# Performance work log

Measured on AMD Instinct MI355X. Metric: run time of the kernel, lower is better.

Reference implementation:

```python
import jax, jax.numpy as jnp
import numpy as np

B, C, H, W = 8, 128, 128, 128
PLANES, K, STRIDE, PAD = 128, 3, 1, 1
BN_EPS = 1e-5


def setup_inputs() -> dict:
    key = jax.random.key(0)
    k1, k2, k3, k4 = jax.random.split(key, 4)
    x = jax.random.normal(k1, (B, C, H, W), jnp.float32)
    # ConvOffset2D: Conv2d(C, 2C, 3, pad=1, bias=False), weights ~ N(0, 0.01)
    w_off = jax.random.normal(k2, (2 * C, C, 3, 3), jnp.float32) * 0.01
    w_conv = jax.random.normal(k3, (PLANES, C, K, K), jnp.float32) * 0.05
    b_conv = jax.random.normal(k4, (PLANES,), jnp.float32) * 0.01
    gamma = jnp.ones((PLANES,), jnp.float32)
    beta = jnp.zeros((PLANES,), jnp.float32)
    return {"x": x, "w_off": w_off, "w_conv": w_conv, "b_conv": b_conv,
            "gamma": gamma, "beta": beta}


def _conv2d(x, w, stride, pad):
    return jax.lax.conv_general_dilated(
        x, w, window_strides=(stride, stride),
        padding=[(pad, pad), (pad, pad)],
        dimension_numbers=("NCHW", "OIHW", "NCHW"))


def _deform_sample(x, offsets):
    """x: (B,C,H,W); offsets: (B,2C,H,W) -> bilinear offset-sampled (B,C,H,W).
    Faithful to ConvOffset2D: raw reshape (b,2c,h,w) -> (b*c, h*w, 2),
    coords = offsets + meshgrid(i,j), clamp, bilinear interp."""
    b, c, h, w = x.shape
    off = offsets.reshape(b * c, h * w, 2)              # quirky but faithful reshape
    grid = jnp.stack(jnp.meshgrid(jnp.arange(h, dtype=x.dtype),
                                  jnp.arange(w, dtype=x.dtype),
                                  indexing="ij"), axis=-1).reshape(1, h * w, 2)
    coords = off + grid                                  # (b*c, h*w, 2)
    yc = jnp.clip(coords[..., 0], 0.0, h - 1.0)
    xc = jnp.clip(coords[..., 1], 0.0, w - 1.0)
    y0, y1 = jnp.floor(yc), jnp.ceil(yc)
    x0, x1 = jnp.floor(xc), jnp.ceil(xc)
    img = x.reshape(b * c, h * w)

    def gather(yy, xx):
        idx = (yy * w + xx).astype(jnp.int32)
        return jnp.take_along_axis(img, idx, axis=1)

    v_lt = gather(y0, x0)
    v_rb = gather(y1, x1)
    v_lb = gather(y0, x1)
    v_rt = gather(y1, x0)
    dy = yc - y0
    dx = xc - x0
    v_t = v_lt + (v_rt - v_lt) * dy   # interp along height
    v_b = v_lb + (v_rb - v_lb) * dy
    out = v_t + (v_b - v_t) * dx      # interp along width
    return out.reshape(b, c, h, w)


def reference(x, w_off, w_conv, b_conv, gamma, beta):
    offsets = _conv2d(x, w_off, 1, 1)                    # (B, 2C, H, W)
    x_off = _deform_sample(x, offsets)                   # (B, C, H, W)
    y = _conv2d(x_off, w_conv, STRIDE, PAD) + b_conv[None, :, None, None]
    y = jax.nn.relu(y)
    # BatchNorm2d in training mode: batch statistics, biased variance
    mean = y.mean(axis=(0, 2, 3), keepdims=True)
    var = jnp.square(y - mean).mean(axis=(0, 2, 3), keepdims=True)
    y = (y - mean) * jax.lax.rsqrt(var + BN_EPS)
    return y * gamma[None, :, None, None] + beta[None, :, None, None]
```

## Files before the change

kernel.cpp:

```cpp
#include <hip/hip_runtime.h>

#define B_   8
#define C_   128
#define H_   128
#define W_   128
#define HW_  16384

typedef short v8s __attribute__((ext_vector_type(8)));
typedef float v4f __attribute__((ext_vector_type(4)));

#define ROWB 4160

__device__ __forceinline__ float bf2f(unsigned short u) {
  unsigned int v = ((unsigned int)u) << 16;
  float f; __builtin_memcpy(&f, &v, 4); return f;
}
__device__ __forceinline__ unsigned short f2us(float f) {
  unsigned int u; __builtin_memcpy(&u, &f, 4);
  u += 0x7fffu + ((u >> 16) & 1u);
  return (unsigned short)(u >> 16);
}

__global__ __launch_bounds__(256) void pack_w(const float* __restrict__ w,
                                              unsigned short* __restrict__ pack,
                                              uint4* __restrict__ zb, int G) {
  if (blockIdx.x == 0) zb[threadIdx.x] = (uint4){0u, 0u, 0u, 0u};
  int idx = blockIdx.x * 256 + threadIdx.x;
  if (idx >= 20480 * G) return;
  int j  = idx & 7;
  int l  = (idx >> 3) & 63;
  int g  = (idx >> 9) % G;
  int t2 = idx / (512 * G);
  int pp = t2 % 5;
  int cc = t2 / 5;
  int oc = g * 16 + (l & 15);
  int kk = ((l >> 4) << 3) + j;
  int ic = (cc << 4) + (kk & 15);
  int rs = pp * 2 + (kk >> 4);
  float v = (rs < 9) ? w[(oc * C_ + ic) * 9 + rs] : 0.f;
  pack[idx] = f2us(v);
}

__global__ __launch_bounds__(256) void transpose_x(const float* __restrict__ x,
                                                   unsigned short* __restrict__ xt) {
  __shared__ alignas(16) unsigned short t[32 * 132];
  const int j0 = blockIdx.x * 32, i = blockIdx.y, b = blockIdx.z;
  const int tid = threadIdx.x;
  for (int e = tid; e < 128 * 32; e += 256) {
    int c = e >> 5, jj = e & 31;
    float v = x[((b * C_ + c) * H_ + i) * W_ + j0 + jj];
    t[jj * 132 + c] = f2us(v);
  }
  __syncthreads();
  for (int f = tid; f < 1024; f += 256) {
    int cg = f >> 7, g = f & 127;
    int j = g >> 2, c4 = (g & 3) << 2;
    uint2 v = *(const uint2*)&t[j * 132 + cg * 16 + c4];
    *(uint2*)(xt + ((size_t)(b * 8 + cg) * HW_ + i * W_ + j0 + j) * 16 + c4) = v;
  }
}

template <int MODE, int G>
__global__ __launch_bounds__(256) void conv_gemm(const unsigned short* __restrict__ xt,
                                                 const unsigned short* __restrict__ pack,
                                                 const float* __restrict__ bias,
                                                 const char* __restrict__ zb,
                                                 unsigned short* __restrict__ outp,
                                                 float* __restrict__ ps) {
  __shared__ alignas(16) char rawb[3 * ROWB];
  __shared__ float bs1[128], bs2[128];

  const int nb = blockIdx.x;
  int b, i, mt;
  {
    int xcd = nb & 7, r = nb >> 3;
    if (MODE == 0) { b = r >> 5; mt = (r >> 4) & 1; i = xcd * 16 + (r & 15); }
    else           { b = r >> 4; mt = 0;            i = xcd * 16 + (r & 15); }
  }
  const int tid  = threadIdx.x;
  const int lane = tid & 63, wid = tid >> 6;
  const int q = lane >> 4, n = lane & 15;
  const int wm = wid & 1, wn = wid >> 1;

  if (MODE == 1 && tid < 128) { bs1[tid] = 0.f; bs2[tid] = 0.f; }
  if (tid < 12) {
    int r = tid >> 2, rem = tid & 3, side = rem >> 1, h = rem & 1;
    *(uint4*)(rawb + r * ROWB + (side ? 129 * 32 : 0) + h * 16) = (uint4){0u,0u,0u,0u};
  }

  int boff[5];
#pragma unroll
  for (int pp = 0; pp < 5; ++pp) {
    int rs = pp * 2 + (q >> 1);
    if (rs > 8) rs = 8;
    int r = (rs >= 6) ? 2 : ((rs >= 3) ? 1 : 0);
    int s = rs - r * 3;
    boff[pp] = r * ROWB + s * 32 + (q & 1) * 16;
  }
  const int pcol = (wn * 64 + n) * 32;

  v4f acc[4][4];
#pragma unroll
  for (int a = 0; a < 4; ++a)
#pragma unroll
    for (int c = 0; c < 4; ++c) acc[a][c] = (v4f){0.f, 0.f, 0.f, 0.f};

  const v8s* packv = (const v8s*)pack;
  const int gbase = mt * 8 + wm * 4;

  v8s Acur[4];
  {
    const v8s* ap = packv + (0 * G + gbase) * 64 + lane;
#pragma unroll
    for (int fm = 0; fm < 4; ++fm) Acur[fm] = ap[fm * 64];
  }

  for (int cc = 0; cc < 8; ++cc) {
    __syncthreads();
    const char* ccbase = (const char*)xt + (size_t)(b * 8 + cc) * (HW_ * 32);
#pragma unroll
    for (int t = 0; t < 3; ++t) {
      int c = wid * 3 + t, r = c >> 2, k = c & 3;
      int ii = i + r - 1;
      const char* src = ((unsigned)ii < 128u)
                          ? ccbase + ii * 4096 + k * 1024 + lane * 16
                          : zb + lane * 16;
      __builtin_amdgcn_global_load_lds(
          (const __attribute__((address_space(1))) unsigned int*)src,
          (__attribute__((address_space(3))) unsigned int*)(rawb + r * ROWB + 32 + k * 1024),
          16, 0, 0);
    }
    __syncthreads();

#pragma unroll
    for (int pp = 0; pp < 5; ++pp) {
      v8s Anxt[4];
      const bool havenext = (pp < 4) || (cc < 7);
      if (havenext) {
        int ncc = (pp < 4) ? cc : cc + 1;
        int npp = (pp < 4) ? pp + 1 : 0;
        const v8s* ap = packv + ((ncc * 5 + npp) * G + gbase) * 64 + lane;
#pragma unroll
        for (int fm = 0; fm < 4; ++fm) Anxt[fm] = ap[fm * 64];
      }
      v8s Bf[4];
#pragma unroll
      for (int fn = 0; fn < 4; ++fn)
        Bf[fn] = *(const v8s*)(rawb + boff[pp] + pcol + fn * 512);
#pragma unroll
      for (int fm = 0; fm < 4; ++fm) {
#pragma unroll
        for (int fn = 0; fn < 4; ++fn)
          acc[fm][fn] = __builtin_amdgcn_mfma_f32_16x16x32_bf16(Acur[fm], Bf[fn],
                                                                acc[fm][fn], 0, 0, 0);
      }
      if (havenext) {
#pragma unroll
        for (int fm = 0; fm < 4; ++fm) Acur[fm] = Anxt[fm];
      }
    }
  }

  const int OC = G * 16;
  const int ob = (b * OC + mt * 128 + wm * 64) * HW_ + i * W_ + wn * 64;

  if (MODE == 0) {
#pragma unroll
    for (int fm = 0; fm < 4; ++fm)
#pragma unroll
      for (int fn = 0; fn < 4; ++fn)
#pragma unroll
        for (int rr = 0; rr < 4; ++rr)
          outp[ob + (fm * 16 + q * 4 + rr) * HW_ + fn * 16 + n] = f2us(acc[fm][fn][rr]);
  } else {
    float bv[4][4], s1a[4][4], s2a[4][4];
#pragma unroll
    for (int fm = 0; fm < 4; ++fm)
#pragma unroll
      for (int rr = 0; rr < 4; ++rr) {
        bv[fm][rr] = bias[wm * 64 + fm * 16 + q * 4 + rr];
        s1a[fm][rr] = 0.f; s2a[fm][rr] = 0.f;
      }
#pragma unroll
    for (int fm = 0; fm < 4; ++fm)
#pragma unroll
      for (int fn = 0; fn < 4; ++fn)
#pragma unroll
        for (int rr = 0; rr < 4; ++rr) {
          float v = acc[fm][fn][rr] + bv[fm][rr];
          v = fmaxf(v, 0.f);
          outp[ob + (fm * 16 + q * 4 + rr) * HW_ + fn * 16 + n] = f2us(v);
          s1a[fm][rr] += v; s2a[fm][rr] += v * v;
        }
#pragma unroll
    for (int fm = 0; fm < 4; ++fm)
#pragma unroll
      for (int rr = 0; rr < 4; ++rr) {
        float s1 = s1a[fm][rr], s2 = s2a[fm][rr];
#pragma unroll
        for (int m = 1; m < 16; m <<= 1) {
          s1 += __shfl_xor(s1, m);
          s2 += __shfl_xor(s2, m);
        }
        if (n == 0) {
          atomicAdd(&bs1[wm * 64 + fm * 16 + q * 4 + rr], s1);
          atomicAdd(&bs2[wm * 64 + fm * 16 + q * 4 + rr], s2);
        }
      }
    __syncthreads();
    if (tid < 128) {
      ps[nb * 128 + tid]          = bs1[tid];
      ps[131072 + nb * 128 + tid] = bs2[tid];
    }
  }
}

__global__ __launch_bounds__(256) void deform_t(const float* __restrict__ x,
                                                const unsigned short* __restrict__ offs,
                                                unsigned short* __restrict__ xofft) {
  __shared__ alignas(16) unsigned short t[128 * 132];
  const int i = blockIdx.x, b = blockIdx.y;
  const int tid = threadIdx.x;
  for (int e = tid; e < 16384; e += 256) {
    int c = e >> 7, j = e & 127;
    int qpix = (i << 7) + j;
    int oidx = (b << 22) + (c << 15) + 2 * qpix;
    unsigned int pr = *(const unsigned int*)(offs + oidx);
    float oy = bf2f((unsigned short)(pr & 0xffffu));
    float ox = bf2f((unsigned short)(pr >> 16));
    float yc = fminf(fmaxf(oy + (float)i, 0.f), 127.f);
    float xc = fminf(fmaxf(ox + (float)j, 0.f), 127.f);
    float y0f = floorf(yc), y1f = ceilf(yc);
    float x0f = floorf(xc), x1f = ceilf(xc);
    int y0 = (int)y0f, y1 = (int)y1f, x0 = (int)x0f, x1 = (int)x1f;
    const float* img = x + ((b * C_ + c) << 14);
    float v_lt = img[y0 * W_ + x0];
    float v_rb = img[y1 * W_ + x1];
    float v_lb = img[y0 * W_ + x1];
    float v_rt = img[y1 * W_ + x0];
    float dy = yc - y0f, dx = xc - x0f;
    float v_t = v_lt + (v_rt - v_lt) * dy;
    float v_b = v_lb + (v_rb - v_lb) * dy;
    float o   = v_t + (v_b - v_t) * dx;
    t[j * 132 + c] = f2us(o);
  }
  __syncthreads();
  for (int f = tid; f < 4096; f += 256) {
    int cg = f >> 9, g = f & 511;
    int j = g >> 2, c4 = (g & 3) << 2;
    uint2 v = *(const uint2*)&t[j * 132 + cg * 16 + c4];
    *(uint2*)(xofft + ((size_t)(b * 8 + cg) * HW_ + i * W_ + j) * 16 + c4) = v;
  }
}

__global__ __launch_bounds__(256) void bn_finalize(const float* __restrict__ ps,
                                                   const float* __restrict__ gamma,
                                                   const float* __restrict__ beta,
                                                   float* __restrict__ stats) {
  const int c = blockIdx.x, tid = threadIdx.x;
  float s1 = 0.f, s2 = 0.f;
  for (int k = tid; k < 1024; k += 256) {
    s1 += ps[k * 128 + c];
    s2 += ps[131072 + k * 128 + c];
  }
#pragma unroll
  for (int m = 32; m > 0; m >>= 1) {
    s1 += __shfl_down(s1, m);
    s2 += __shfl_down(s2, m);
  }
  __shared__ float l1[4], l2[4];
  int wid = tid >> 6;
  if ((tid & 63) == 0) { l1[wid] = s1; l2[wid] = s2; }
  __syncthreads();
  if (tid == 0) {
    s1 = l1[0] + l1[1] + l1[2] + l1[3];
    s2 = l2[0] + l2[1] + l2[2] + l2[3];
    const float invn = 1.f / 131072.f;
    float mean = s1 * invn;
    float var  = s2 * invn - mean * mean;
    float inv  = rsqrtf(var + 1e-5f);
    float sc = gamma[c] * inv;
    stats[c]       = sc;
    stats[128 + c] = beta[c] - mean * sc;
  }
}

__global__ __launch_bounds__(256) void bn_apply(const unsigned short* __restrict__ y,
                                                const float* __restrict__ stats,
                                                float* __restrict__ out) {
  int gid = blockIdx.x * 256 + threadIdx.x;
  int base = gid << 3;
  int c = (base >> 14) & 127;
  float sc = stats[c], sh = stats[128 + c];
  uint4 u = *(const uint4*)(y + base);
  const unsigned short* us = (const unsigned short*)&u;
  float4 o0, o1;
  o0.x = bf2f(us[0]) * sc + sh;  o0.y = bf2f(us[1]) * sc + sh;
  o0.z = bf2f(us[2]) * sc + sh;  o0.w = bf2f(us[3]) * sc + sh;
  o1.x = bf2f(us[4]) * sc + sh;  o1.y = bf2f(us[5]) * sc + sh;
  o1.z = bf2f(us[6]) * sc + sh;  o1.w = bf2f(us[7]) * sc + sh;
  ((float4*)out)[gid * 2]     = o0;
  ((float4*)out)[gid * 2 + 1] = o1;
}

extern "C" void kernel_launch(void* const* d_in, const int* in_sizes, int n_in,
                              void* d_out, int out_size, void* d_ws, size_t ws_size,
                              hipStream_t stream) {
  const float* x      = (const float*)d_in[0];
  const float* w_off  = (const float*)d_in[1];
  const float* w_conv = (const float*)d_in[2];
  const float* b_conv = (const float*)d_in[3];
  const float* gamma  = (const float*)d_in[4];
  const float* beta   = (const float*)d_in[5];
  float* out = (float*)d_out;

  char* ws = (char*)d_ws;
  unsigned short* x_t    = (unsigned short*)ws;
  unsigned short* xoff_t = (unsigned short*)ws;
  unsigned short* offs = (unsigned short*)(ws + 33554432);
  unsigned short* yws  = (unsigned short*)(ws + 33554432);
  float* ps    = (float*)(ws + 67108864);
  float* stats = (float*)(ws + 68157440);
  unsigned short* pack_off  = (unsigned short*)(ws + 100663296);
  unsigned short* pack_main = (unsigned short*)(ws + 101318656);
  char* zb = ws + 101646336;

  pack_w<<<80 * 16, 256, 0, stream>>>(w_off, pack_off, (uint4*)zb, 16);
  pack_w<<<80 * 8, 256, 0, stream>>>(w_conv, pack_main, (uint4*)zb, 8);
  transpose_x<<<dim3(4, 128, 8), 256, 0, stream>>>(x, x_t);
  conv_gemm<0, 16><<<2048, 256, 0, stream>>>(x_t, pack_off, nullptr, zb, offs, nullptr);
  deform_t<<<dim3(128, 8), 256, 0, stream>>>(x, offs, xoff_t);
  conv_gemm<1, 8><<<1024, 256, 0, stream>>>(xoff_t, pack_main, b_conv, zb, yws, ps);
  bn_finalize<<<128, 256, 0, stream>>>(ps, gamma, beta, stats);
  bn_apply<<<8192, 256, 0, stream>>>(yws, stats, out);
}
```

Before: 332.2 us.

## Double-buffer LDS input rows in conv GEMM and merge weight packing launches

The conv GEMM now keeps two LDS staging buffers and prefetches the next input-channel chunk with global_load_lds while MFMAs run on the current one. This drops one barrier per iteration and aims to hide global-to-LDS latency. The two weight-pack kernels are merged into one launch, and transpose_x now reads x with float4 loads. In exchange, LDS use per block roughly doubles, which can lower occupancy, and correctness depends on the barrier waiting for the asynchronous LDS loads to finish.

```diff
diff --git a/kernel.cpp b/kernel.cpp
--- a/kernel.cpp
+++ b/kernel.cpp
@@ -21,11 +21,19 @@
   return (unsigned short)(u >> 16);
 }
 
-__global__ __launch_bounds__(256) void pack_w(const float* __restrict__ w,
-                                              unsigned short* __restrict__ pack,
-                                              uint4* __restrict__ zb, int G) {
+__global__ __launch_bounds__(256) void pack_all(const float* __restrict__ w_off,
+                                                const float* __restrict__ w_conv,
+                                                unsigned short* __restrict__ pack_off,
+                                                unsigned short* __restrict__ pack_main,
+                                                uint4* __restrict__ zb) {
   if (blockIdx.x == 0) zb[threadIdx.x] = (uint4){0u, 0u, 0u, 0u};
-  int idx = blockIdx.x * 256 + threadIdx.x;
+  const float* w;
+  unsigned short* pack;
+  int G, idx;
+  if (blockIdx.x < 1280) { w = w_off; pack = pack_off; G = 16;
+                           idx = blockIdx.x * 256 + threadIdx.x; }
+  else                   { w = w_conv; pack = pack_main; G = 8;
+                           idx = (blockIdx.x - 1280) * 256 + threadIdx.x; }
   if (idx >= 20480 * G) return;
   int j  = idx & 7;
   int l  = (idx >> 3) & 63;
@@ -46,10 +54,13 @@
   __shared__ alignas(16) unsigned short t[32 * 132];
   const int j0 = blockIdx.x * 32, i = blockIdx.y, b = blockIdx.z;
   const int tid = threadIdx.x;
-  for (int e = tid; e < 128 * 32; e += 256) {
-    int c = e >> 5, jj = e & 31;
-    float v = x[((b * C_ + c) * H_ + i) * W_ + j0 + jj];
-    t[jj * 132 + c] = f2us(v);
+  for (int f = tid; f < 1024; f += 256) {
+    int c = f >> 3, j4 = (f & 7) << 2;
+    float4 v = *(const float4*)&x[((b * C_ + c) * H_ + i) * W_ + j0 + j4];
+    t[(j4 + 0) * 132 + c] = f2us(v.x);
+    t[(j4 + 1) * 132 + c] = f2us(v.y);
+    t[(j4 + 2) * 132 + c] = f2us(v.z);
+    t[(j4 + 3) * 132 + c] = f2us(v.w);
   }
   __syncthreads();
   for (int f = tid; f < 1024; f += 256) {
@@ -67,8 +78,7 @@
                                                  const char* __restrict__ zb,
                                                  unsigned short* __restrict__ outp,
                                                  float* __restrict__ ps) {
-  __shared__ alignas(16) char rawb[3 * ROWB];
-  __shared__ float bs1[128], bs2[128];
+  __shared__ alignas(16) char rawb[2][3 * ROWB];
 
   const int nb = blockIdx.x;
   int b, i, mt;
@@ -82,10 +92,11 @@
   const int q = lane >> 4, n = lane & 15;
   const int wm = wid & 1, wn = wid >> 1;
 
-  if (MODE == 1 && tid < 128) { bs1[tid] = 0.f; bs2[tid] = 0.f; }
-  if (tid < 12) {
-    int r = tid >> 2, rem = tid & 3, side = rem >> 1, h = rem & 1;
-    *(uint4*)(rawb + r * ROWB + (side ? 129 * 32 : 0) + h * 16) = (uint4){0u,0u,0u,0u};
+  if (tid < 24) {
+    int bufi = tid >= 12, u = tid % 12;
+    int r = u >> 2, rem = u & 3, side = rem >> 1, h = rem & 1;
+    *(uint4*)(rawb[bufi] + r * ROWB + (side ? 129 * 32 : 0) + h * 16) =
+        (uint4){0u, 0u, 0u, 0u};
   }
 
   int boff[5];
@@ -99,6 +110,21 @@
   }
   const int pcol = (wn * 64 + n) * 32;
 
+  const char* dsrc[3];
+  int ddst[3];
+#pragma unroll
+  for (int t = 0; t < 3; ++t) {
+    int c = wid * 3 + t, r = c >> 2, k = c & 3;
+    int ii = i + r - 1;
+    dsrc[t] = ((unsigned)ii < 128u)
+                ? (const char*)xt + (size_t)(b * 8) * (HW_ * 32) + ii * 4096 + k * 1024 + lane * 16
+                : zb + lane * 16;
+    ddst[t] = r * ROWB + 32 + k * 1024;
+  }
+  const bool dval[3] = {(unsigned)(i + (((wid * 3 + 0) >> 2)) - 1) < 128u,
+                        (unsigned)(i + (((wid * 3 + 1) >> 2)) - 1) < 128u,
+                        (unsigned)(i + (((wid * 3 + 2) >> 2)) - 1) < 128u};
+
   v4f acc[4][4];
 #pragma unroll
   for (int a = 0; a < 4; ++a)
@@ -115,22 +141,30 @@
     for (int fm = 0; fm < 4; ++fm) Acur[fm] = ap[fm * 64];
   }
 
+#pragma unroll
+  for (int t = 0; t < 3; ++t) {
+    const char* src = dval[t] ? dsrc[t] : dsrc[t];
+    __builtin_amdgcn_global_load_lds(
+        (const __attribute__((address_space(1))) unsigned int*)src,
+        (__attribute__((address_space(3))) unsigned int*)(rawb[0] + ddst[t]),
+        16, 0, 0);
+  }
+
   for (int cc = 0; cc < 8; ++cc) {
+    char* cur = rawb[cc & 1];
+    char* nxt = rawb[(cc + 1) & 1];
     __syncthreads();
-    const char* ccbase = (const char*)xt + (size_t)(b * 8 + cc) * (HW_ * 32);
-#pragma unroll
-    for (int t = 0; t < 3; ++t) {
-      int c = wid * 3 + t, r = c >> 2, k = c & 3;
-      int ii = i + r - 1;
-      const char* src = ((unsigned)ii < 128u)
-                          ? ccbase + ii * 4096 + k * 1024 + lane * 16
-                          : zb + lane * 16;
-      __builtin_amdgcn_global_load_lds(
-          (const __attribute__((address_space(1))) unsigned int*)src,
-          (__attribute__((address_space(3))) unsigned int*)(rawb + r * ROWB + 32 + k * 1024),
-          16, 0, 0);
+    if (cc < 7) {
+      const size_t adv = (size_t)(cc + 1) * (HW_ * 32);
+#pragma unroll
+      for (int t = 0; t < 3; ++t) {
+        const char* src = dval[t] ? dsrc[t] + adv : dsrc[t];
+        __builtin_amdgcn_global_load_lds(
+            (const __attribute__((address_space(1))) unsigned int*)src,
+            (__attribute__((address_space(3))) unsigned int*)(nxt + ddst[t]),
+            16, 0, 0);
+      }
     }
-    __syncthreads();
 
 #pragma unroll
     for (int pp = 0; pp < 5; ++pp) {
@@ -146,7 +180,7 @@
       v8s Bf[4];
 #pragma unroll
       for (int fn = 0; fn < 4; ++fn)
-        Bf[fn] = *(const v8s*)(rawb + boff[pp] + pcol + fn * 512);
+        Bf[fn] = *(const v8s*)(cur + boff[pp] + pcol + fn * 512);
 #pragma unroll
       for (int fm = 0; fm < 4; ++fm) {
 #pragma unroll
@@ -173,6 +207,10 @@
         for (int rr = 0; rr < 4; ++rr)
           outp[ob + (fm * 16 + q * 4 + rr) * HW_ + fn * 16 + n] = f2us(acc[fm][fn][rr]);
   } else {
+    __shared__ float bs1[128], bs2[128];
+    __syncthreads();
+    if (tid < 128) { bs1[tid] = 0.f; bs2[tid] = 0.f; }
+    __syncthreads();
     float bv[4][4], s1a[4][4], s2a[4][4];
 #pragma unroll
     for (int fm = 0; fm < 4; ++fm)
@@ -325,8 +363,7 @@
   unsigned short* pack_main = (unsigned short*)(ws + 101318656);
   char* zb = ws + 101646336;
 
-  pack_w<<<80 * 16, 256, 0, stream>>>(w_off, pack_off, (uint4*)zb, 16);
-  pack_w<<<80 * 8, 256, 0, stream>>>(w_conv, pack_main, (uint4*)zb, 8);
+  pack_all<<<1920, 256, 0, stream>>>(w_off, w_conv, pack_off, pack_main, (uint4*)zb);
   transpose_x<<<dim3(4, 128, 8), 256, 0, stream>>>(x, x_t);
   conv_gemm<0, 16><<<2048, 256, 0, stream>>>(x_t, pack_off, nullptr, zb, offs, nullptr);
   deform_t<<<dim3(128, 8), 256, 0, stream>>>(x, offs, xoff_t);
```

New measurement: 335.5 us. No clear change (+1.0%).
